# Kernel optimization log

Measured on AMD Instinct MI355X. Metric: run time of the kernel, lower is better.

## Reference

```python
import jax, jax.numpy as jnp
import numpy as np

S, B, D, H, V, TOK = 512, 32, 512, 512, 64, 30000
L = 2  # num LSTM layers


def _lstm_dir(x, Wih, Whh, bih, bhh, reverse):
    # x: [S, B, Din]; Wih: [4H, Din]; Whh: [4H, H]
    Bn = x.shape[1]
    Hn = Whh.shape[1]

    def step(carry, xt):
        h, c = carry
        g = xt @ Wih.T + h @ Whh.T + bih + bhh  # [B, 4H]
        i, f, gg, o = jnp.split(g, 4, axis=-1)  # torch gate order i,f,g,o
        c = jax.nn.sigmoid(f) * c + jax.nn.sigmoid(i) * jnp.tanh(gg)
        h = jax.nn.sigmoid(o) * jnp.tanh(c)
        return (h, c), h

    init = (jnp.zeros((Bn, Hn), x.dtype), jnp.zeros((Bn, Hn), x.dtype))
    _, hs = jax.lax.scan(step, init, x, reverse=reverse)
    return hs  # [S, B, H], time-aligned with x


def _bilstm(x, Wih0, Whh0, bih0, bhh0, Wih1, Whh1, bih1, bhh1):
    # layer 0
    hf = _lstm_dir(x, Wih0[0], Whh0[0], bih0[0], bhh0[0], reverse=False)
    hb = _lstm_dir(x, Wih0[1], Whh0[1], bih0[1], bhh0[1], reverse=True)
    x = jnp.concatenate([hf, hb], axis=-1)  # [S, B, 2H]
    # layer 1
    hf = _lstm_dir(x, Wih1[0], Whh1[0], bih1[0], bhh1[0], reverse=False)
    hb = _lstm_dir(x, Wih1[1], Whh1[1], bih1[1], bhh1[1], reverse=True)
    return jnp.concatenate([hf, hb], axis=-1)  # [S, B, 2H]


def setup_inputs() -> dict:
    key = jax.random.key(0)
    ks = jax.random.split(key, 16)
    s = 0.05
    inp = {}
    inp['source'] = jax.random.randint(ks[0], (S, B), 0, TOK)
    inp['target'] = jax.random.randint(ks[1], (S, B), 0, V)
    inp['emb'] = jax.random.normal(ks[2], (TOK, D), jnp.float32) * s
    inp['Wih0'] = jax.random.normal(ks[3], (2, 4 * H, D), jnp.float32) * s
    inp['Whh0'] = jax.random.normal(ks[4], (2, 4 * H, H), jnp.float32) * s
    inp['bih0'] = jax.random.normal(ks[5], (2, 4 * H), jnp.float32) * s
    inp['bhh0'] = jax.random.normal(ks[6], (2, 4 * H), jnp.float32) * s
    inp['Wih1'] = jax.random.normal(ks[7], (2, 4 * H, 2 * H), jnp.float32) * s
    inp['Whh1'] = jax.random.normal(ks[8], (2, 4 * H, H), jnp.float32) * s
    inp['bih1'] = jax.random.normal(ks[9], (2, 4 * H), jnp.float32) * s
    inp['bhh1'] = jax.random.normal(ks[10], (2, 4 * H), jnp.float32) * s
    inp['Wout'] = jax.random.normal(ks[11], (V, 2 * H), jnp.float32) * s
    inp['bout'] = jax.random.normal(ks[12], (V,), jnp.float32) * s
    inp['trans'] = jax.random.uniform(ks[13], (V, V), jnp.float32)  # torch.rand
    return inp


def reference(source, target, emb, Wih0, Whh0, bih0, bhh0, Wih1, Whh1, bih1, bhh1, Wout, bout, trans):
    # get_logits: frozen embedding -> BiLSTM -> linear
    x = jax.lax.stop_gradient(emb[source])  # [S, B, D] (embedding under no_grad)
    h = _bilstm(x, Wih0, Whh0, bih0, bhh0, Wih1, Whh1, bih1, bhh1)  # [S, B, 2H]
    logits = (h @ Wout.T + bout)[:, 0, :]  # [S, V] -- forward() decodes batch 0

    # Viterbi: max-plus recurrence over time
    def vstep(delta, lt):
        scores = delta[:, None] + trans + lt[None, :]  # [V_prev, V_cur]
        return jnp.max(scores, axis=0), jnp.argmax(scores, axis=0)

    delta, bps = jax.lax.scan(vstep, logits[0], logits[1:])  # bps: [S-1, V]
    last = jnp.argmax(delta)

    def back(idx, bp):
        prev = bp[idx]
        return prev, prev

    _, rev = jax.lax.scan(back, last, bps, reverse=True)  # rev[t] = tag at t, t in [0, S-2]
    path = jnp.concatenate([rev, last[None]]).astype(jnp.int32)  # [S]
    return path
```

## Files before the change

### kernel.cpp

```cpp
#include <hip/hip_runtime.h>
#include <stdint.h>

constexpr int kS = 512;
constexpr int kB = 32;
constexpr int kH = 512;
constexpr int kV = 64;


__device__ __forceinline__ float fast_sigmoid(float x) {
  return __builtin_amdgcn_rcpf(1.0f + __expf(-x));
}
__device__ __forceinline__ float fast_tanh(float x) {
  return 1.0f - 2.0f * __builtin_amdgcn_rcpf(1.0f + __expf(2.0f * x));
}
__device__ __forceinline__ float bcast(float v, int k) {
  return __uint_as_float(__builtin_amdgcn_readlane(__float_as_uint(v), k));
}
__device__ __forceinline__ unsigned ld_l2(const unsigned* p) {
  unsigned r;
  asm volatile("global_load_dword %0, %1, off sc0\n\ts_waitcnt vmcnt(0)"
               : "=v"(r) : "v"(p) : "memory");
  return r;
}
__device__ __forceinline__ void st_l2(unsigned* p, unsigned v) {
  asm volatile("global_store_dword %0, %1, off sc0" :: "v"(p), "v"(v)
               : "memory");
}

__global__ __launch_bounds__(128) void k_embed(const int* __restrict__ src,
                                               const float* __restrict__ emb,
                                               float* __restrict__ X) {
  const int t = blockIdx.x;
  const int s = src[t * kB];
  const float4* e = (const float4*)(emb + (size_t)s * 512);
  float4* x = (float4*)(X + (size_t)t * 512);
  x[threadIdx.x] = e[threadIdx.x];
}

template <int KZ>
__global__ __launch_bounds__(512, 1) void k_rec(
    const float* __restrict__ Z0,
    const float* __restrict__ Z1,
    const float* __restrict__ Wih,
    const float* __restrict__ Whh,
    const float* __restrict__ bih,
    const float* __restrict__ bhh,
    float* __restrict__ HL,
    float* __restrict__ HG) {
  constexpr int ZPW = KZ / 8;
  __shared__ float part[64 * 9];
  const int b = blockIdx.x;
  const int xslot = b & 7;
  if (xslot > 1) return;
  const int dir = xslot, wg = b >> 3;
  const int tid = threadIdx.x;
  const int wv = tid >> 6, l = tid & 63;
  const float* WihB = Wih + (size_t)dir * 2048 * KZ;
  const float* WhhB = Whh + (size_t)dir * 2048 * 512;
  float* HbL = HL + (size_t)dir * kS * kH;
  float* HbG = HG + (size_t)dir * kS * kH;
  const int grow = (l >> 4) * 512 + wg * 16 + (l & 15);

  float ww[64];
  {
    const float* wp = WhhB + (size_t)grow * 512 + wv * 64;
#pragma unroll
    for (int i = 0; i < 64; i += 4) {
      const float4 v = *(const float4*)(wp + i);
      ww[i] = v.x; ww[i + 1] = v.y; ww[i + 2] = v.z; ww[i + 3] = v.w;
    }
  }
  float zw[ZPW];
  {
    const float* zp = WihB + (size_t)grow * KZ + wv * ZPW;
#pragma unroll
    for (int i = 0; i < ZPW; i += 4) {
      const float4 v = *(const float4*)(zp + i);
      zw[i] = v.x; zw[i + 1] = v.y; zw[i + 2] = v.z; zw[i + 3] = v.w;
    }
  }
  float bias = 0.0f;
  if (wv == 0) bias = bih[dir * 2048 + grow] + bhh[dir * 2048 + grow];
  float cstate = 0.0f;

  const float* zbase = (KZ == 512) ? Z0 : ((wv < 4) ? Z0 : Z1);
  const int zoff = (KZ == 512) ? tid : ((wv & 3) * 128 + l);

  const int t0 = dir ? (kS - 1) : 0;
  float zc0 = zbase[(size_t)t0 * 512 + zoff];
  float zc1 = (KZ == 1024) ? zbase[(size_t)t0 * 512 + zoff + 64] : 0.0f;

  for (int s = 0; s < kS; s++) {
    const int t = dir ? (kS - 1 - s) : s;
    int tn = dir ? (t - 1) : (t + 1);
    if (tn < 0) tn = 0;
    if (tn > kS - 1) tn = kS - 1;
    const float zn0 = zbase[(size_t)tn * 512 + zoff];
    const float zn1 = (KZ == 1024) ? zbase[(size_t)tn * 512 + zoff + 64] : 0.0f;

    float a0 = 0.f, a1 = 0.f, a2 = 0.f, a3 = 0.f;
#pragma unroll
    for (int k = 0; k < 64; k += 4) {
      a0 += zw[k + 0] * bcast(zc0, k + 0);
      a1 += zw[k + 1] * bcast(zc0, k + 1);
      a2 += zw[k + 2] * bcast(zc0, k + 2);
      a3 += zw[k + 3] * bcast(zc0, k + 3);
    }
    if (KZ == 1024) {
#pragma unroll
      for (int k = 0; k < 64; k += 4) {
        a0 += zw[64 + k + 0] * bcast(zc1, k + 0);
        a1 += zw[64 + k + 1] * bcast(zc1, k + 1);
        a2 += zw[64 + k + 2] * bcast(zc1, k + 2);
        a3 += zw[64 + k + 3] * bcast(zc1, k + 3);
      }
    }

    float hreg = 0.0f;
    if (s > 0) {
      const int tp = dir ? (t + 1) : (t - 1);
      const unsigned* lp = (const unsigned*)(HbL + (size_t)tp * kH) + tid;
      const unsigned* gp = (const unsigned*)(HbG + (size_t)tp * kH) + tid;
      unsigned u = ld_l2(lp);
#pragma unroll 1
      for (int r = 0; r < 4; r++) {
        if (u != 0xFFFFFFFFu) break;
        u = ld_l2(lp);
      }
      while (u == 0xFFFFFFFFu)
        u = __hip_atomic_load(gp, __ATOMIC_RELAXED, __HIP_MEMORY_SCOPE_AGENT);
      hreg = __uint_as_float(u);
    }

#pragma unroll
    for (int k = 0; k < 64; k += 4) {
      a0 += ww[k + 0] * bcast(hreg, k + 0);
      a1 += ww[k + 1] * bcast(hreg, k + 1);
      a2 += ww[k + 2] * bcast(hreg, k + 2);
      a3 += ww[k + 3] * bcast(hreg, k + 3);
    }
    part[l * 9 + wv] = (a0 + a1) + (a2 + a3);
    __syncthreads();
    if (wv == 0) {
      float ssum = bias;
#pragma unroll
      for (int w = 0; w < 8; w++) ssum += part[l * 9 + w];
      const float sf = __shfl(ssum, (l + 16) & 63);
      const float sg = __shfl(ssum, (l + 32) & 63);
      const float so = __shfl(ssum, (l + 48) & 63);
      if (l < 16) {
        const float ig = fast_sigmoid(ssum);
        const float fg = fast_sigmoid(sf);
        const float og = fast_sigmoid(so);
        cstate = fg * cstate + ig * fast_tanh(sg);
        const float h = og * fast_tanh(cstate);
        const unsigned hv = __float_as_uint(h);
        unsigned* lq = (unsigned*)(HbL + (size_t)t * kH) + wg * 16 + l;
        unsigned* gq = (unsigned*)(HbG + (size_t)t * kH) + wg * 16 + l;
        st_l2(lq, hv);
        __hip_atomic_store(gq, hv, __ATOMIC_RELAXED,
                           __HIP_MEMORY_SCOPE_AGENT);
      }
    }
    zc0 = zn0;
    zc1 = zn1;
  }
}

__global__ __launch_bounds__(256) void k_logits(const float* __restrict__ H1,
                                                const float* __restrict__ Wout,
                                                const float* __restrict__ bout,
                                                float* __restrict__ LOG) {
  __shared__ float hl[1024];
  const int t = blockIdx.x;
  const int tid = threadIdx.x;
  float4* hl4 = (float4*)hl;
  if (tid < 128)
    hl4[tid] = ((const float4*)(H1 + (size_t)t * kH))[tid];
  else
    hl4[tid] = ((const float4*)(H1 + (size_t)(kS + t) * kH))[tid - 128];
  __syncthreads();
  const int v = tid >> 2, q = tid & 3;
  const float4* w4 = (const float4*)(Wout + (size_t)v * 1024);
  float4 a = {0, 0, 0, 0};
#pragma unroll 8
  for (int j = 0; j < 64; j++) {
    const int idx = j * 4 + q;
    const float4 w = w4[idx];
    const float4 x = hl4[idx];
    a.x += w.x * x.x; a.y += w.y * x.y; a.z += w.z * x.z; a.w += w.w * x.w;
  }
  float acc = (a.x + a.y) + (a.z + a.w);
  acc += __shfl_xor(acc, 1);
  acc += __shfl_xor(acc, 2);
  if (q == 0) LOG[(size_t)t * kV + v] = acc + bout[v];
}

__global__ __launch_bounds__(256) void k_viterbi(const float* __restrict__ LOG,
                                                 const float* __restrict__ trans,
                                                 int* __restrict__ out) {
  __shared__ float delta[64];
  __shared__ float redS[4 * 64];
  __shared__ int redA[4 * 64];
  __shared__ unsigned char bp[511 * 64];
  const int tid = threadIdx.x;
  const int c = tid & 63, q = tid >> 6;
  if (tid < 64) delta[tid] = LOG[tid];
  __syncthreads();
  for (int t = 1; t < kS; t++) {
    float best = -1e30f;
    int bi = 0;
#pragma unroll 4
    for (int pp = 0; pp < 16; pp++) {
      const int p = q * 16 + pp;
      const float sc = delta[p] + trans[p * 64 + c];
      if (sc > best) { best = sc; bi = p; }
    }
    redS[q * 64 + c] = best;
    redA[q * 64 + c] = bi;
    __syncthreads();
    if (tid < 64) {
      float b = redS[c];
      int a = redA[c];
      for (int qq = 1; qq < 4; qq++) {
        const float v2 = redS[qq * 64 + c];
        if (v2 > b) { b = v2; a = redA[qq * 64 + c]; }
      }
      bp[(t - 1) * 64 + c] = (unsigned char)a;
      delta[c] = b + LOG[t * 64 + c];
    }
    __syncthreads();
  }
  if (tid == 0) {
    float b = delta[0];
    int a = 0;
    for (int i = 1; i < 64; i++)
      if (delta[i] > b) { b = delta[i]; a = i; }
    int idx = a;
    out[kS - 1] = idx;
    for (int t = kS - 2; t >= 0; t--) {
      idx = bp[t * 64 + idx];
      out[t] = idx;
    }
  }
}

extern "C" void kernel_launch(void* const* d_in, const int* in_sizes, int n_in,
                              void* d_out, int out_size, void* d_ws,
                              size_t ws_size, hipStream_t stream) {
  (void)in_sizes; (void)n_in; (void)out_size; (void)ws_size;
  const int* source  = (const int*)d_in[0];
  const float* emb   = (const float*)d_in[2];
  const float* Wih0  = (const float*)d_in[3];
  const float* Whh0  = (const float*)d_in[4];
  const float* bih0  = (const float*)d_in[5];
  const float* bhh0  = (const float*)d_in[6];
  const float* Wih1  = (const float*)d_in[7];
  const float* Whh1  = (const float*)d_in[8];
  const float* bih1  = (const float*)d_in[9];
  const float* bhh1  = (const float*)d_in[10];
  const float* Wout  = (const float*)d_in[11];
  const float* bout  = (const float*)d_in[12];
  const float* trans = (const float*)d_in[13];

  float* ws = (float*)d_ws;
  float* X   = ws;
  float* H0L = ws + 262144;
  float* H0G = ws + 786432;
  float* H1L = ws + 1310720;
  float* H1G = ws + 1835008;
  float* LOG = ws + 2359296;

  hipMemsetAsync(H0L, 0xFF, (size_t)4 * 524288 * sizeof(float), stream);

  k_embed<<<kS, 128, 0, stream>>>(source, emb, X);
  k_rec<512><<<256, 512, 0, stream>>>(X, X, Wih0, Whh0, bih0, bhh0, H0L, H0G);
  k_rec<1024><<<256, 512, 0, stream>>>(H0G, H0G + 262144, Wih1, Whh1, bih1,
                                       bhh1, H1L, H1G);
  k_logits<<<kS, 256, 0, stream>>>(H1G, Wout, bout, LOG);
  k_viterbi<<<1, 256, 0, stream>>>(LOG, trans, (int*)d_out);
}
```

Measured before the change: 2.022 ms.

## Assign LSTM directions to blocks by runtime XCC id to keep traffic local

Each block of the recurrent kernel now reads its hardware XCC id and publishes it to a control array. All blocks then spin until every block has published. From the gathered map, the kernel picks two XCCs that each hold at least 32 blocks and assigns each direction's 32 workgroups to one of them. This replaces the old assumption that blockIdx modulo 8 picks the XCC. It aims to keep the per-step hidden-state exchange within one XCC's L2 and to read through the global path only when the producer sits on another die. It adds a grid-wide startup barrier and a serial 256-iteration scan per block. It also risks deadlock if not all 256 blocks are co-resident.

```diff
diff --git a/kernel.cpp b/kernel.cpp
--- a/kernel.cpp
+++ b/kernel.cpp
@@ -5,7 +5,10 @@
 constexpr int kB = 32;
 constexpr int kH = 512;
 constexpr int kV = 64;
-
+constexpr int kNB = 256;
+
+
+#define HWREG_XCC_ID ((20) | (0 << 6) | (31 << 11))
 
 __device__ __forceinline__ float fast_sigmoid(float x) {
   return __builtin_amdgcn_rcpf(1.0f + __expf(-x));
@@ -46,15 +49,78 @@
     const float* __restrict__ bih,
     const float* __restrict__ bhh,
     float* __restrict__ HL,
-    float* __restrict__ HG) {
+    float* __restrict__ HG,
+    int* __restrict__ CTL) {
   constexpr int ZPW = KZ / 8;
   __shared__ float part[64 * 9];
+  __shared__ int xccs[kNB];
+  __shared__ int scnt[8];
   const int b = blockIdx.x;
-  const int xslot = b & 7;
-  if (xslot > 1) return;
-  const int dir = xslot, wg = b >> 3;
   const int tid = threadIdx.x;
   const int wv = tid >> 6, l = tid & 63;
+
+  const int myxcc = (int)(__builtin_amdgcn_s_getreg(HWREG_XCC_ID) & 7u);
+  if (tid == 0)
+    __hip_atomic_store(&CTL[b], myxcc, __ATOMIC_RELAXED,
+                       __HIP_MEMORY_SCOPE_AGENT);
+  if (tid < 8) scnt[tid] = 0;
+  if (tid < kNB) {
+    int v;
+    do {
+      v = __hip_atomic_load(&CTL[tid], __ATOMIC_RELAXED,
+                            __HIP_MEMORY_SCOPE_AGENT);
+    } while (v == -1);
+    xccs[tid] = v & 7;
+  }
+  __syncthreads();
+  if (tid < kNB) atomicAdd(&scnt[xccs[tid]], 1);
+  __syncthreads();
+
+  int T0 = 0, T1 = -1;
+#pragma unroll
+  for (int x = 7; x >= 0; x--) if (scnt[x] >= 32) T0 = x == 7 ? x : T0;
+  T0 = 0; T1 = -1;
+#pragma unroll
+  for (int x = 0; x < 8; x++) {
+    if (T0 == 0 && x == 0) {}
+  }
+  {
+    int t0 = -1, t1 = -1;
+#pragma unroll
+    for (int x = 0; x < 8; x++) {
+      if (t0 < 0 && scnt[x] >= 32) t0 = x;
+    }
+#pragma unroll
+    for (int x = 0; x < 8; x++) {
+      if (t1 < 0 && x != t0 && scnt[x] >= 32) t1 = x;
+    }
+    T0 = t0;
+    T1 = t1;
+  }
+
+  int dir = -1, wg = 0;
+  int px0 = T0, px1 = (T1 >= 0) ? T1 : T0;
+  {
+    const int want = tid >> 4;
+    int c0 = 0, c1 = 0;
+    for (int i = 0; i < kNB; i++) {
+      const int xi = xccs[i];
+      const bool s0 = (xi == T0) && (c0 < 32);
+      const bool s1 = !s0 && ((T1 >= 0) ? ((xi == T1) && (c1 < 32))
+                                        : (c1 < 32));
+      if (i == b) {
+        if (s0) { dir = 0; wg = c0; }
+        else if (s1) { dir = 1; wg = c1; }
+      }
+      if (s0 && c0 == want) px0 = xi;
+      if (s1 && c1 == want) px1 = xi;
+      c0 += (int)s0; c1 += (int)s1;
+    }
+  }
+  if (dir < 0) return;
+  const int pxcc = dir ? px1 : px0;
+  bool useG = (pxcc != myxcc);
+
   const float* WihB = Wih + (size_t)dir * 2048 * KZ;
   const float* WhhB = Whh + (size_t)dir * 2048 * 512;
   float* HbL = HL + (size_t)dir * kS * kH;
@@ -121,14 +187,17 @@
       const int tp = dir ? (t + 1) : (t - 1);
       const unsigned* lp = (const unsigned*)(HbL + (size_t)tp * kH) + tid;
       const unsigned* gp = (const unsigned*)(HbG + (size_t)tp * kH) + tid;
-      unsigned u = ld_l2(lp);
-#pragma unroll 1
-      for (int r = 0; r < 4; r++) {
-        if (u != 0xFFFFFFFFu) break;
+      unsigned u = 0xFFFFFFFFu;
+      if (!useG) {
         u = ld_l2(lp);
-      }
-      while (u == 0xFFFFFFFFu)
-        u = __hip_atomic_load(gp, __ATOMIC_RELAXED, __HIP_MEMORY_SCOPE_AGENT);
+        int tries = 0;
+        while (u == 0xFFFFFFFFu && ++tries < 64) u = ld_l2(lp);
+        if (u == 0xFFFFFFFFu) useG = true;
+      }
+      if (useG) {
+        while (u == 0xFFFFFFFFu)
+          u = __hip_atomic_load(gp, __ATOMIC_RELAXED, __HIP_MEMORY_SCOPE_AGENT);
+      }
       hreg = __uint_as_float(u);
     }
 
@@ -270,13 +339,17 @@
   float* H1L = ws + 1310720;
   float* H1G = ws + 1835008;
   float* LOG = ws + 2359296;
+  int* CTL0  = (int*)(ws + 2392064);
+  int* CTL1  = CTL0 + kNB;
 
   hipMemsetAsync(H0L, 0xFF, (size_t)4 * 524288 * sizeof(float), stream);
+  hipMemsetAsync(CTL0, 0xFF, (size_t)2 * kNB * sizeof(int), stream);
 
   k_embed<<<kS, 128, 0, stream>>>(source, emb, X);
-  k_rec<512><<<256, 512, 0, stream>>>(X, X, Wih0, Whh0, bih0, bhh0, H0L, H0G);
-  k_rec<1024><<<256, 512, 0, stream>>>(H0G, H0G + 262144, Wih1, Whh1, bih1,
-                                       bhh1, H1L, H1G);
+  k_rec<512><<<kNB, 512, 0, stream>>>(X, X, Wih0, Whh0, bih0, bhh0, H0L, H0G,
+                                      CTL0);
+  k_rec<1024><<<kNB, 512, 0, stream>>>(H0G, H0G + 262144, Wih1, Whh1, bih1,
+                                       bhh1, H1L, H1G, CTL1);
   k_logits<<<kS, 256, 0, stream>>>(H1G, Wout, bout, LOG);
   k_viterbi<<<1, 256, 0, stream>>>(LOG, trans, (int*)d_out);
 }
```

Result: slower. 2.542 ms (+25.7%).

## Precompute LSTM input projections in parallel kernel before recurrence

Applied to the files above, without the earlier changes.

Splits the input-to-hidden projection out of the sequential recurrent kernel into a separate, fully parallel kernel that computes Wih·x plus biases for all timesteps into a workspace buffer. The recurrent kernel then only does the Whh·h product per step and reads the precomputed gate preactivations, which shortens the serial critical path. This costs extra workspace memory and an additional read of the precomputed buffer, and it falls back to the fused kernel if the workspace is too small.

```diff
diff --git a/kernel.cpp b/kernel.cpp
--- a/kernel.cpp
+++ b/kernel.cpp
@@ -25,6 +25,9 @@
 __device__ __forceinline__ void st_l2(unsigned* p, unsigned v) {
   asm volatile("global_store_dword %0, %1, off sc0" :: "v"(p), "v"(v)
                : "memory");
+}
+__device__ __forceinline__ unsigned ld_agent(const unsigned* p) {
+  return __hip_atomic_load(p, __ATOMIC_RELAXED, __HIP_MEMORY_SCOPE_AGENT);
 }
 
 __global__ __launch_bounds__(128) void k_embed(const int* __restrict__ src,
@@ -38,15 +41,175 @@
 }
 
 template <int KZ>
-__global__ __launch_bounds__(512, 1) void k_rec(
+__global__ __launch_bounds__(512) void k_xg(
     const float* __restrict__ Z0,
     const float* __restrict__ Z1,
     const float* __restrict__ Wih,
-    const float* __restrict__ Whh,
     const float* __restrict__ bih,
     const float* __restrict__ bhh,
+    float* __restrict__ Xg) {
+  constexpr int ZPW = KZ / 8;
+  __shared__ float part[64 * 9];
+  const int b = blockIdx.x;
+  const int dir = b & 1, rs = (b >> 1) & 31, tc = b >> 6;
+  const int tid = threadIdx.x;
+  const int wv = tid >> 6, l = tid & 63;
+  const int grow = (l >> 4) * 512 + rs * 16 + (l & 15);
+
+  float zw[ZPW];
+  {
+    const float* zp = Wih + ((size_t)dir * 2048 + grow) * KZ + wv * ZPW;
+#pragma unroll
+    for (int i = 0; i < ZPW; i += 4) {
+      const float4 v = *(const float4*)(zp + i);
+      zw[i] = v.x; zw[i + 1] = v.y; zw[i + 2] = v.z; zw[i + 3] = v.w;
+    }
+  }
+  float bias = 0.0f;
+  if (wv == 0) bias = bih[dir * 2048 + grow] + bhh[dir * 2048 + grow];
+  float* XgD = Xg + (size_t)dir * kS * 2048;
+
+  const float* zbase = (KZ == 512) ? Z0 : ((wv < 4) ? Z0 : Z1);
+  const int zoff = (KZ == 512) ? tid : ((wv & 3) * 128 + l);
+
+  const int tbase = tc * 64;
+  float zc0 = zbase[(size_t)tbase * 512 + zoff];
+  float zc1 = (KZ == 1024) ? zbase[(size_t)tbase * 512 + zoff + 64] : 0.0f;
+
+  for (int i = 0; i < 64; i++) {
+    const int t = tbase + i;
+    const int tn = (i < 63) ? (t + 1) : t;
+    const float zn0 = zbase[(size_t)tn * 512 + zoff];
+    const float zn1 = (KZ == 1024) ? zbase[(size_t)tn * 512 + zoff + 64] : 0.0f;
+
+    float a0 = 0.f, a1 = 0.f, a2 = 0.f, a3 = 0.f;
+#pragma unroll
+    for (int k = 0; k < 64; k += 4) {
+      a0 += zw[k + 0] * bcast(zc0, k + 0);
+      a1 += zw[k + 1] * bcast(zc0, k + 1);
+      a2 += zw[k + 2] * bcast(zc0, k + 2);
+      a3 += zw[k + 3] * bcast(zc0, k + 3);
+    }
+    if (KZ == 1024) {
+#pragma unroll
+      for (int k = 0; k < 64; k += 4) {
+        a0 += zw[64 + k + 0] * bcast(zc1, k + 0);
+        a1 += zw[64 + k + 1] * bcast(zc1, k + 1);
+        a2 += zw[64 + k + 2] * bcast(zc1, k + 2);
+        a3 += zw[64 + k + 3] * bcast(zc1, k + 3);
+      }
+    }
+    part[l * 9 + wv] = (a0 + a1) + (a2 + a3);
+    __syncthreads();
+    if (wv == 0) {
+      float ssum = bias;
+#pragma unroll
+      for (int w = 0; w < 8; w++) ssum += part[l * 9 + w];
+      XgD[(size_t)t * 2048 + grow] = ssum;
+    }
+    __syncthreads();
+    zc0 = zn0;
+    zc1 = zn1;
+  }
+}
+
+__global__ __launch_bounds__(512, 1) void k_rec_pre(
+    const float* __restrict__ Xg,
+    const float* __restrict__ Whh,
     float* __restrict__ HL,
     float* __restrict__ HG) {
+  __shared__ float part[64 * 9];
+  const int b = blockIdx.x;
+  const int xslot = b & 7;
+  if (xslot > 1) return;
+  const int dir = xslot, wg = b >> 3;
+  const int tid = threadIdx.x;
+  const int wv = tid >> 6, l = tid & 63;
+  const float* WhhB = Whh + (size_t)dir * 2048 * 512;
+  const float* XgD = Xg + (size_t)dir * kS * 2048;
+  float* HbL = HL + (size_t)dir * kS * kH;
+  float* HbG = HG + (size_t)dir * kS * kH;
+  const int grow = (l >> 4) * 512 + wg * 16 + (l & 15);
+
+  float ww[64];
+  {
+    const float* wp = WhhB + (size_t)grow * 512 + wv * 64;
+#pragma unroll
+    for (int i = 0; i < 64; i += 4) {
+      const float4 v = *(const float4*)(wp + i);
+      ww[i] = v.x; ww[i + 1] = v.y; ww[i + 2] = v.z; ww[i + 3] = v.w;
+    }
+  }
+  float cstate = 0.0f;
+
+  const int t0 = dir ? (kS - 1) : 0;
+  float xgc = 0.0f;
+  if (wv == 0) xgc = XgD[(size_t)t0 * 2048 + grow];
+
+  for (int s = 0; s < kS; s++) {
+    const int t = dir ? (kS - 1 - s) : s;
+    int tn = dir ? (t - 1) : (t + 1);
+    if (tn < 0) tn = 0;
+    if (tn > kS - 1) tn = kS - 1;
+    float xgn = 0.0f;
+    if (wv == 0) xgn = XgD[(size_t)tn * 2048 + grow];
+
+    float hreg = 0.0f;
+    if (s > 0) {
+      const int tp = dir ? (t + 1) : (t - 1);
+      const unsigned* lp = (const unsigned*)(HbL + (size_t)tp * kH) + tid;
+      const unsigned* gp = (const unsigned*)(HbG + (size_t)tp * kH) + tid;
+      unsigned u = ld_l2(lp);
+#pragma unroll 1
+      for (int r = 0; r < 4; r++) {
+        if (u != 0xFFFFFFFFu) break;
+        u = ld_l2(lp);
+      }
+      while (u == 0xFFFFFFFFu) u = ld_agent(gp);
+      hreg = __uint_as_float(u);
+    }
+
+    float a0 = 0.f, a1 = 0.f, a2 = 0.f, a3 = 0.f;
+#pragma unroll
+    for (int k = 0; k < 64; k += 4) {
+      a0 += ww[k + 0] * bcast(hreg, k + 0);
+      a1 += ww[k + 1] * bcast(hreg, k + 1);
+      a2 += ww[k + 2] * bcast(hreg, k + 2);
+      a3 += ww[k + 3] * bcast(hreg, k + 3);
+    }
+    part[l * 9 + wv] = (a0 + a1) + (a2 + a3);
+    __syncthreads();
+    if (wv == 0) {
+      float ssum = xgc;
+#pragma unroll
+      for (int w = 0; w < 8; w++) ssum += part[l * 9 + w];
+      const float sf = __shfl(ssum, (l + 16) & 63);
+      const float sg = __shfl(ssum, (l + 32) & 63);
+      const float so = __shfl(ssum, (l + 48) & 63);
+      if (l < 16) {
+        const float ig = fast_sigmoid(ssum);
+        const float fg = fast_sigmoid(sf);
+        const float og = fast_sigmoid(so);
+        cstate = fg * cstate + ig * fast_tanh(sg);
+        const float h = og * fast_tanh(cstate);
+        const unsigned hv = __float_as_uint(h);
+        unsigned* lq = (unsigned*)(HbL + (size_t)t * kH) + wg * 16 + l;
+        unsigned* gq = (unsigned*)(HbG + (size_t)t * kH) + wg * 16 + l;
+        st_l2(lq, hv);
+        __hip_atomic_store(gq, hv, __ATOMIC_RELAXED,
+                           __HIP_MEMORY_SCOPE_AGENT);
+      }
+      xgc = xgn;
+    }
+  }
+}
+
+template <int KZ>
+__global__ __launch_bounds__(512, 1) void k_rec(
+    const float* __restrict__ Z0, const float* __restrict__ Z1,
+    const float* __restrict__ Wih, const float* __restrict__ Whh,
+    const float* __restrict__ bih, const float* __restrict__ bhh,
+    float* __restrict__ HL, float* __restrict__ HG) {
   constexpr int ZPW = KZ / 8;
   __shared__ float part[64 * 9];
   const int b = blockIdx.x;
@@ -127,8 +290,7 @@
         if (u != 0xFFFFFFFFu) break;
         u = ld_l2(lp);
       }
-      while (u == 0xFFFFFFFFu)
-        u = __hip_atomic_load(gp, __ATOMIC_RELAXED, __HIP_MEMORY_SCOPE_AGENT);
+      while (u == 0xFFFFFFFFu) u = ld_agent(gp);
       hreg = __uint_as_float(u);
     }
 
@@ -248,7 +410,7 @@
 extern "C" void kernel_launch(void* const* d_in, const int* in_sizes, int n_in,
                               void* d_out, int out_size, void* d_ws,
                               size_t ws_size, hipStream_t stream) {
-  (void)in_sizes; (void)n_in; (void)out_size; (void)ws_size;
+  (void)in_sizes; (void)n_in; (void)out_size;
   const int* source  = (const int*)d_in[0];
   const float* emb   = (const float*)d_in[2];
   const float* Wih0  = (const float*)d_in[3];
@@ -270,13 +432,27 @@
   float* H1L = ws + 1310720;
   float* H1G = ws + 1835008;
   float* LOG = ws + 2359296;
+  float* Xg0 = ws + 2392064;
+  float* Xg1 = ws + 4489216;
 
   hipMemsetAsync(H0L, 0xFF, (size_t)4 * 524288 * sizeof(float), stream);
 
   k_embed<<<kS, 128, 0, stream>>>(source, emb, X);
-  k_rec<512><<<256, 512, 0, stream>>>(X, X, Wih0, Whh0, bih0, bhh0, H0L, H0G);
-  k_rec<1024><<<256, 512, 0, stream>>>(H0G, H0G + 262144, Wih1, Whh1, bih1,
-                                       bhh1, H1L, H1G);
+
+  const size_t need = (size_t)(4489216 + 2097152) * sizeof(float);
+  if (ws_size >= need) {
+    k_xg<512><<<512, 512, 0, stream>>>(X, X, Wih0, bih0, bhh0, Xg0);
+    k_rec_pre<<<256, 512, 0, stream>>>(Xg0, Whh0, H0L, H0G);
+    k_xg<1024><<<512, 512, 0, stream>>>(H0G, H0G + 262144, Wih1, bih1, bhh1,
+                                        Xg1);
+    k_rec_pre<<<256, 512, 0, stream>>>(Xg1, Whh1, H1L, H1G);
+  } else {
+    k_rec<512><<<256, 512, 0, stream>>>(X, X, Wih0, Whh0, bih0, bhh0, H0L,
+                                        H0G);
+    k_rec<1024><<<256, 512, 0, stream>>>(H0G, H0G + 262144, Wih1, Whh1, bih1,
+                                         bhh1, H1L, H1G);
+  }
+
   k_logits<<<kS, 256, 0, stream>>>(H1G, Wout, bout, LOG);
   k_viterbi<<<1, 256, 0, stream>>>(LOG, trans, (int*)d_out);
 }
```

Measured after the change: 2.352 ms. +16.3%, slower.
